# Optimization experiments

Hardware: AMD Instinct MI355X
Metric: run time of the kernel (lower is better)

## Reference

```python
import jax, jax.numpy as jnp
import numpy as np

B = 1024          # number of graphs
H = 8             # heads
EPS = 1e-5        # LayerNorm eps (torch default)
MEAN_RES_SCALE = 0.2


def _ln(x, w, b):
    mu = x.mean(-1, keepdims=True)
    var = ((x - mu) ** 2).mean(-1, keepdims=True)
    return (x - mu) / jnp.sqrt(var + EPS) * w + b


def setup_inputs() -> dict:
    key = jax.random.key(0)
    ks = jax.random.split(key, 10)
    N, D = 262144, 256
    s = 1.0 / np.sqrt(D)
    return {
        "h": jax.random.normal(ks[0], (N, D), jnp.float32),
        "batch": jnp.sort(jax.random.randint(ks[1], (N,), 0, B)),
        "cdr_mask": jax.random.bernoulli(ks[2], 0.2, (N,)),
        "iface_mask": jax.random.bernoulli(ks[3], 0.2, (N,)),
        "ln_kv_w": jnp.ones((D,), jnp.float32),
        "ln_kv_b": jnp.zeros((D,), jnp.float32),
        "ln_q_w": jnp.ones((D,), jnp.float32),
        "ln_q_b": jnp.zeros((D,), jnp.float32),
        "Wk": jax.random.normal(ks[4], (D, D), jnp.float32) * s,
        "Wv": jax.random.normal(ks[5], (D, D), jnp.float32) * s,
        "Wq": jax.random.normal(ks[6], (D, 2 * D), jnp.float32) * (1.0 / np.sqrt(2 * D)),
        "Wres": jax.random.normal(ks[7], (D, D), jnp.float32) * s,
        "Wout": jax.random.normal(ks[8], (D, D), jnp.float32) * s,
        "cdr_bias": jnp.asarray(0.6, jnp.float32),
        "iface_bias": jnp.asarray(0.8, jnp.float32),
        "logit_scale": jnp.asarray(1.0, jnp.float32),
    }


def reference(h, batch, cdr_mask, iface_mask, ln_kv_w, ln_kv_b, ln_q_w, ln_q_b,
              Wk, Wv, Wq, Wres, Wout, cdr_bias, iface_bias, logit_scale):
    N, D = h.shape
    hd = D // H
    # per-graph mean / max pooling (segment reductions; all segments non-empty)
    counts = jax.ops.segment_sum(jnp.ones((N,), h.dtype), batch, num_segments=B)[:, None]
    mean_raw = jax.ops.segment_sum(h, batch, num_segments=B) / counts      # [B,D]
    max_raw = jax.ops.segment_max(h, batch, num_segments=B)                # [B,D]
    # single query per graph (dropout = identity in eval)
    q = jnp.concatenate([mean_raw, max_raw], axis=-1) @ Wq.T               # [B,D]
    q = _ln(q, ln_q_w, ln_q_b).reshape(B, H, hd)                           # [B,H,hd]
    # keys / values per node
    h_ln = _ln(h, ln_kv_w, ln_kv_b)
    k = (h_ln @ Wk.T).reshape(N, H, hd)
    v = (h_ln @ Wv.T).reshape(N, H, hd)
    # attention logits with mask biases
    logit = (k * q[batch]).sum(-1) * (logit_scale / np.sqrt(hd))           # [N,H]
    logit = logit + cdr_bias * cdr_mask.astype(h.dtype)[:, None]
    logit = logit + iface_bias * iface_mask.astype(h.dtype)[:, None]
    # segment softmax over nodes of each graph
    m = jax.ops.segment_max(logit, batch, num_segments=B)                  # [B,H]
    e = jnp.exp(logit - m[batch])
    z = jax.ops.segment_sum(e, batch, num_segments=B)                      # [B,H]
    attn = e / z[batch]                                                    # [N,H]
    g = jax.ops.segment_sum(attn[..., None] * v, batch, num_segments=B)    # [B,H,hd]
    g = g.reshape(B, D)
    return g @ Wout.T + MEAN_RES_SCALE * (mean_raw @ Wres.T)               # [B,D]
```

## Files before the change

kernel.cpp:

```cpp
#include <hip/hip_runtime.h>

__global__ void k_offsets(const int* __restrict__ batch, int* __restrict__ start,
                          int N, int B) {
    int i = blockIdx.x * blockDim.x + threadIdx.x;
    if (i >= N) return;
    int b = batch[i];
    if (i == 0) {
        for (int g = 0; g <= b; ++g) start[g] = 0;
    } else {
        int pb = batch[i - 1];
        for (int g = pb + 1; g <= b; ++g) start[g] = i;
    }
    if (i == N - 1) {
        for (int g = b + 1; g <= B; ++g) start[g] = N;
    }
}

__global__ __launch_bounds__(256) void k_pool_q(
    const float* __restrict__ h, const int* __restrict__ start,
    const float* __restrict__ Wq, const float* __restrict__ Wk,
    const float* __restrict__ ln_q_w, const float* __restrict__ ln_q_b,
    const float* __restrict__ ln_kv_w, const float* __restrict__ logit_scale,
    float* __restrict__ mean_raw, float* __restrict__ w_eff)
{
    const int g = blockIdx.x;
    const int tid = threadIdx.x;
    const int w = tid >> 6;
    const int l = tid & 63;
    const int d = tid;
    const int s = start[g], e = start[g + 1];

    float4 sm = make_float4(0.f, 0.f, 0.f, 0.f);
    float4 mx = make_float4(-INFINITY, -INFINITY, -INFINITY, -INFINITY);
    int n = s + w;
    for (; n + 4 < e; n += 8) {
        const float4 a = *(const float4*)(h + (size_t)n * 256 + l * 4);
        const float4 b = *(const float4*)(h + (size_t)(n + 4) * 256 + l * 4);
        sm.x += a.x + b.x; sm.y += a.y + b.y; sm.z += a.z + b.z; sm.w += a.w + b.w;
        mx.x = fmaxf(mx.x, fmaxf(a.x, b.x)); mx.y = fmaxf(mx.y, fmaxf(a.y, b.y));
        mx.z = fmaxf(mx.z, fmaxf(a.z, b.z)); mx.w = fmaxf(mx.w, fmaxf(a.w, b.w));
    }
    if (n < e) {
        const float4 a = *(const float4*)(h + (size_t)n * 256 + l * 4);
        sm.x += a.x; sm.y += a.y; sm.z += a.z; sm.w += a.w;
        mx.x = fmaxf(mx.x, a.x); mx.y = fmaxf(mx.y, a.y);
        mx.z = fmaxf(mx.z, a.z); mx.w = fmaxf(mx.w, a.w);
    }

    __shared__ __align__(16) float PS[4][256];
    __shared__ __align__(16) float PM[4][256];
    *(float4*)(&PS[w][l * 4]) = sm;
    *(float4*)(&PM[w][l * 4]) = mx;
    __syncthreads();
    const float sum = (PS[0][d] + PS[1][d]) + (PS[2][d] + PS[3][d]);
    const float mxv = fmaxf(fmaxf(PM[0][d], PM[1][d]), fmaxf(PM[2][d], PM[3][d]));
    const float mean = sum / (float)(e - s);
    mean_raw[(size_t)g * 256 + d] = mean;

    __shared__ __align__(16) float X[512];
    __shared__ float QL[256];
    __shared__ float rs[4], rq[4];
    X[d] = mean;
    X[256 + d] = mxv;
    __syncthreads();

    float q = 0.f;
    const float* wqr = Wq + (size_t)d * 512;
    #pragma unroll 8
    for (int j = 0; j < 512; j += 4) {
        float4 w4 = *(const float4*)(wqr + j);
        q += w4.x * X[j] + w4.y * X[j + 1] + w4.z * X[j + 2] + w4.w * X[j + 3];
    }
    float s1 = q, s2 = q * q;
    #pragma unroll
    for (int off = 1; off < 64; off <<= 1) {
        s1 += __shfl_xor(s1, off);
        s2 += __shfl_xor(s2, off);
    }
    if ((d & 63) == 0) { rs[d >> 6] = s1; rq[d >> 6] = s2; }
    __syncthreads();
    const float t1 = rs[0] + rs[1] + rs[2] + rs[3];
    const float t2 = rq[0] + rq[1] + rq[2] + rq[3];
    const float mu = t1 * (1.f / 256.f);
    const float var = t2 * (1.f / 256.f) - mu * mu;
    const float rstd = rsqrtf(var + 1e-5f);
    QL[d] = (q - mu) * rstd * ln_q_w[d] + ln_q_b[d];
    __syncthreads();

    const float scale = logit_scale[0] * 0.17677669529663687f;
    const float fold = scale * ln_kv_w[d];
    #pragma unroll
    for (int hh = 0; hh < 8; ++hh) {
        float a = 0.f;
        #pragma unroll 8
        for (int r = 0; r < 32; ++r) {
            a += Wk[(size_t)(hh * 32 + r) * 256 + d] * QL[hh * 32 + r];
        }
        w_eff[((size_t)g * 8 + hh) * 256 + d] = a * fold;
    }
}

__global__ __launch_bounds__(256) void k_attn(
    const float* __restrict__ h, const int* __restrict__ start,
    const int* __restrict__ cdr, const int* __restrict__ ifm,
    const float* __restrict__ ln_w, const float* __restrict__ ln_b,
    const float* __restrict__ w_eff,
    const float* __restrict__ cdr_bias, const float* __restrict__ iface_bias,
    float* __restrict__ u_norm)
{
    const int g = blockIdx.x;
    const int tid = threadIdx.x;
    const int w = tid >> 6;
    const int l = tid & 63;
    const int hh = l >> 3;
    const int p = l & 7;
    const int s = start[g], e = start[g + 1];
    const float cb = cdr_bias[0], ib = iface_bias[0];

    float we[32];
    {
        const float* wp = w_eff + ((size_t)g * 8 + hh) * 256 + p * 32;
        #pragma unroll
        for (int r = 0; r < 8; ++r) {
            float4 t = *(const float4*)(wp + r * 4);
            we[4 * r + 0] = t.x; we[4 * r + 1] = t.y; we[4 * r + 2] = t.z; we[4 * r + 3] = t.w;
        }
    }
    float s1h = 0.f;
    #pragma unroll
    for (int r = 0; r < 32; ++r) s1h += we[r];
    s1h += __shfl_xor(s1h, 1);
    s1h += __shfl_xor(s1h, 2);
    s1h += __shfl_xor(s1h, 4);

    float m = -INFINITY, z = 0.f, sw = 0.f;
    float u[32];
    #pragma unroll
    for (int r = 0; r < 32; ++r) u[r] = 0.f;

    __shared__ __align__(16) float hbuf[4][288];
    __shared__ __align__(16) float UF[4][8][264];
    __shared__ float MW[4][8], ZW[4][8], SW[4][8], FG[4][8], IZ[8], SG[8];

    const int wofs = l * 4 + ((l >> 3) << 2);
    const int rofs = p * 36;

    int n = s + w;
    float4 xn = make_float4(0.f, 0.f, 0.f, 0.f);
    int cn = 0, im = 0;
    if (n < e) {
        xn = *(const float4*)(h + (size_t)n * 256 + l * 4);
        cn = cdr[n]; im = ifm[n];
    }
    while (n < e) {
        const float4 xc = xn;
        const int cc = cn, ic = im;
        const int n2 = n + 4;
        if (n2 < e) {
            xn = *(const float4*)(h + (size_t)n2 * 256 + l * 4);
            cn = cdr[n2]; im = ifm[n2];
        }

        *(float4*)(&hbuf[w][wofs]) = xc;
        asm volatile("s_waitcnt lgkmcnt(0)" ::: "memory");

        float hv[32];
        #pragma unroll
        for (int r = 0; r < 8; ++r) {
            float4 t = *(const float4*)(&hbuf[w][rofs + r * 4]);
            hv[4 * r + 0] = t.x; hv[4 * r + 1] = t.y; hv[4 * r + 2] = t.z; hv[4 * r + 3] = t.w;
        }
        float s1 = 0.f, s2 = 0.f, dt = 0.f;
        #pragma unroll
        for (int r = 0; r < 32; ++r) {
            const float v = hv[r];
            s1 += v;
            s2 = fmaf(v, v, s2);
            dt = fmaf(v, we[r], dt);
        }
        #pragma unroll
        for (int off = 1; off < 8; off <<= 1) {
            s1 += __shfl_xor(s1, off);
            s2 += __shfl_xor(s2, off);
            dt += __shfl_xor(dt, off);
        }
        const float mu = s1 * (1.f / 256.f);
        const float var = s2 * (1.f / 256.f) - mu * mu;
        const float rstd = rsqrtf(var + 1e-5f);
        const float mb = cb * (float)cc + ib * (float)ic;
        const float lv = rstd * (dt - mu * s1h) + mb;

        const float nm = fmaxf(m, lv);
        const float ee = __expf(lv - nm);
        const float c = ee * rstd;
        if (__any(lv > m)) {
            const float a = __expf(m - nm);
            z = z * a + ee;
            sw = sw * a + c * mu;
            #pragma unroll
            for (int r = 0; r < 32; ++r) u[r] = u[r] * a + c * hv[r];
            m = nm;
        } else {
            z += ee;
            sw += c * mu;
            #pragma unroll
            for (int r = 0; r < 32; ++r) u[r] = fmaf(c, hv[r], u[r]);
        }
        n = n2;
    }

    if (p == 0) { MW[w][hh] = m; ZW[w][hh] = z; SW[w][hh] = sw; }
    #pragma unroll
    for (int r = 0; r < 8; ++r) {
        float4 t = make_float4(u[4 * r], u[4 * r + 1], u[4 * r + 2], u[4 * r + 3]);
        *(float4*)(&UF[w][hh][p * 32 + r * 4]) = t;
    }
    __syncthreads();

    if (tid < 8) {
        const float mg = fmaxf(fmaxf(MW[0][tid], MW[1][tid]),
                               fmaxf(MW[2][tid], MW[3][tid]));
        float zg = 0.f, sg = 0.f;
        #pragma unroll
        for (int ww = 0; ww < 4; ++ww) {
            const float f = __expf(MW[ww][tid] - mg);
            FG[ww][tid] = f;
            zg += ZW[ww][tid] * f;
            sg += SW[ww][tid] * f;
        }
        IZ[tid] = 1.f / zg;
        SG[tid] = sg;
    }
    __syncthreads();

    const float lwj = ln_w[tid], lbj = ln_b[tid];
    #pragma unroll
    for (int h2 = 0; h2 < 8; ++h2) {
        const float Uv = UF[0][h2][tid] * FG[0][h2] + UF[1][h2][tid] * FG[1][h2]
                       + UF[2][h2][tid] * FG[2][h2] + UF[3][h2][tid] * FG[3][h2];
        u_norm[(size_t)g * 2048 + h2 * 256 + tid] = (Uv - SG[h2]) * IZ[h2] * lwj + lbj;
    }
}

__global__ __launch_bounds__(256) void k_out(
    const float* __restrict__ u_norm, const float* __restrict__ mean_raw,
    const float* __restrict__ Wv, const float* __restrict__ Wout,
    const float* __restrict__ Wres, float* __restrict__ out)
{
    const int d = threadIdx.x;
    const int g = blockIdx.x;
    __shared__ __align__(16) float UN[8][256];
    __shared__ __align__(16) float MR[256];
    __shared__ __align__(16) float GF[256];

    const float4* up = (const float4*)(u_norm + (size_t)g * 2048);
    ((float4*)UN)[d] = up[d];
    ((float4*)UN)[256 + d] = up[256 + d];
    if (d < 64) ((float4*)MR)[d] = ((const float4*)(mean_raw + (size_t)g * 256))[d];
    __syncthreads();

    const int hh = d >> 5;
    float acc = 0.f;
    const float* wvr = Wv + (size_t)d * 256;
    #pragma unroll 8
    for (int j = 0; j < 256; j += 4) {
        const float4 wv = *(const float4*)(wvr + j);
        const float4 uv = *(const float4*)(&UN[hh][j]);
        acc += wv.x * uv.x + wv.y * uv.y + wv.z * uv.z + wv.w * uv.w;
    }
    GF[d] = acc;
    __syncthreads();

    float oo = 0.f, rr = 0.f;
    const float* wor = Wout + (size_t)d * 256;
    const float* wrr = Wres + (size_t)d * 256;
    #pragma unroll 8
    for (int j = 0; j < 256; j += 4) {
        const float4 wo = *(const float4*)(wor + j);
        const float4 wq = *(const float4*)(wrr + j);
        const float4 gf = *(const float4*)(&GF[j]);
        const float4 mr = *(const float4*)(&MR[j]);
        oo += wo.x * gf.x + wo.y * gf.y + wo.z * gf.z + wo.w * gf.w;
        rr += wq.x * mr.x + wq.y * mr.y + wq.z * mr.z + wq.w * mr.w;
    }
    out[(size_t)g * 256 + d] = oo + 0.2f * rr;
}

extern "C" void kernel_launch(void* const* d_in, const int* in_sizes, int n_in,
                              void* d_out, int out_size, void* d_ws, size_t ws_size,
                              hipStream_t stream)
{
    const float* h        = (const float*)d_in[0];
    const int*   batch    = (const int*)d_in[1];
    const int*   cdr      = (const int*)d_in[2];
    const int*   ifm      = (const int*)d_in[3];
    const float* ln_kv_w  = (const float*)d_in[4];
    const float* ln_kv_b  = (const float*)d_in[5];
    const float* ln_q_w   = (const float*)d_in[6];
    const float* ln_q_b   = (const float*)d_in[7];
    const float* Wk       = (const float*)d_in[8];
    const float* Wv       = (const float*)d_in[9];
    const float* Wq       = (const float*)d_in[10];
    const float* Wres     = (const float*)d_in[11];
    const float* Wout     = (const float*)d_in[12];
    const float* cdr_b    = (const float*)d_in[13];
    const float* if_b     = (const float*)d_in[14];
    const float* lsc      = (const float*)d_in[15];

    const int N = in_sizes[0] / 256;
    const int B = out_size / 256;

    int*   start    = (int*)d_ws;
    float* mean_raw = (float*)((char*)d_ws + 8192);
    float* w_eff    = mean_raw + (size_t)B * 256;
    float* u_norm   = w_eff + (size_t)B * 2048;

    k_offsets<<<(N + 255) / 256, 256, 0, stream>>>(batch, start, N, B);
    k_pool_q<<<B, 256, 0, stream>>>(h, start, Wq, Wk, ln_q_w, ln_q_b, ln_kv_w, lsc,
                                    mean_raw, w_eff);
    k_attn<<<B, 256, 0, stream>>>(h, start, cdr, ifm, ln_kv_w, ln_kv_b, w_eff,
                                  cdr_b, if_b, u_norm);
    k_out<<<B, 256, 0, stream>>>(u_norm, mean_raw, Wv, Wout, Wres, (float*)d_out);
}
```

Baseline: 669.6 us.

## Split pooling into node-chunked atomic kernel, precompute mask bias, deepen attn prefetch

Mean/max pooling moves out of the per-graph q kernel into a separate kernel over fixed 128-node chunks. It accumulates per-graph partial sums and maxes with float atomicAdd and an ordered-int atomicMax, so load balance no longer depends on segment sizes. The mask bias is precomputed per node in the offsets kernel, and the attention loop now prefetches three rows ahead instead of one. This adds an init kernel, atomic traffic and extra launches, and float atomic summation makes the mean order-nondeterministic.

```diff
diff --git a/kernel.cpp b/kernel.cpp
--- a/kernel.cpp
+++ b/kernel.cpp
@@ -1,9 +1,27 @@
 #include <hip/hip_runtime.h>
 
-__global__ void k_offsets(const int* __restrict__ batch, int* __restrict__ start,
+__device__ __forceinline__ int okey(float x) {
+    int ix = __float_as_int(x);
+    return ix >= 0 ? ix : (ix ^ 0x7fffffff);
+}
+__device__ __forceinline__ float okey_dec(int k) {
+    return __int_as_float(k >= 0 ? k : (k ^ 0x7fffffff));
+}
+
+__global__ __launch_bounds__(256) void k_init(float* __restrict__ gsum,
+                                              int* __restrict__ gmax, int total) {
+    int i = blockIdx.x * blockDim.x + threadIdx.x;
+    if (i < total) { gsum[i] = 0.f; gmax[i] = (int)0x80000000; }
+}
+
+__global__ void k_offsets(const int* __restrict__ batch, const int* __restrict__ cdr,
+                          const int* __restrict__ ifm, const float* __restrict__ cdr_bias,
+                          const float* __restrict__ iface_bias,
+                          int* __restrict__ start, float* __restrict__ mbias,
                           int N, int B) {
     int i = blockIdx.x * blockDim.x + threadIdx.x;
     if (i >= N) return;
+    mbias[i] = cdr_bias[0] * (float)cdr[i] + iface_bias[0] * (float)ifm[i];
     int b = batch[i];
     if (i == 0) {
         for (int g = 0; g <= b; ++g) start[g] = 0;
@@ -16,45 +34,73 @@
     }
 }
 
-__global__ __launch_bounds__(256) void k_pool_q(
-    const float* __restrict__ h, const int* __restrict__ start,
+__global__ __launch_bounds__(256) void k_pool(
+    const float* __restrict__ h, const int* __restrict__ batch,
+    float* __restrict__ gsum, int* __restrict__ gmax, int N)
+{
+    const int c0 = blockIdx.x * 128;
+    const int tid = threadIdx.x;
+    const int w = tid >> 6;
+    const int l = tid & 63;
+    const int lim = min(128, N - c0);
+
+    __shared__ int bb[128];
+    if (tid < 128 && c0 + tid < N) bb[tid] = batch[c0 + tid];
+    __syncthreads();
+
+    float4 sm = make_float4(0.f, 0.f, 0.f, 0.f);
+    float4 mxv = make_float4(-INFINITY, -INFINITY, -INFINITY, -INFINITY);
+
+    const bool any = (w < lim);
+    int cur = any ? bb[w] : 0;
+
+    auto flush = [&](int g2) {
+        float* sp = gsum + ((size_t)g2 << 8) + (l << 2);
+        atomicAdd(sp + 0, sm.x); atomicAdd(sp + 1, sm.y);
+        atomicAdd(sp + 2, sm.z); atomicAdd(sp + 3, sm.w);
+        int* mp = gmax + ((size_t)g2 << 8) + (l << 2);
+        atomicMax(mp + 0, okey(mxv.x)); atomicMax(mp + 1, okey(mxv.y));
+        atomicMax(mp + 2, okey(mxv.z)); atomicMax(mp + 3, okey(mxv.w));
+    };
+
+    float4 xa = make_float4(0.f, 0.f, 0.f, 0.f);
+    float4 xb = make_float4(0.f, 0.f, 0.f, 0.f);
+    if (w < lim)     xa = *(const float4*)(h + (size_t)(c0 + w) * 256 + l * 4);
+    if (w + 4 < lim) xb = *(const float4*)(h + (size_t)(c0 + w + 4) * 256 + l * 4);
+
+    for (int idx = w; idx < lim; idx += 4) {
+        const float4 xc = xa;
+        xa = xb;
+        if (idx + 8 < lim)
+            xb = *(const float4*)(h + (size_t)(c0 + idx + 8) * 256 + l * 4);
+        const int bg = bb[idx];
+        if (bg != cur) {
+            flush(cur);
+            sm = make_float4(0.f, 0.f, 0.f, 0.f);
+            mxv = make_float4(-INFINITY, -INFINITY, -INFINITY, -INFINITY);
+            cur = bg;
+        }
+        sm.x += xc.x; sm.y += xc.y; sm.z += xc.z; sm.w += xc.w;
+        mxv.x = fmaxf(mxv.x, xc.x); mxv.y = fmaxf(mxv.y, xc.y);
+        mxv.z = fmaxf(mxv.z, xc.z); mxv.w = fmaxf(mxv.w, xc.w);
+    }
+    if (any) flush(cur);
+}
+
+__global__ __launch_bounds__(256) void k_q(
+    const float* __restrict__ gsum, const int* __restrict__ gmax,
+    const int* __restrict__ start,
     const float* __restrict__ Wq, const float* __restrict__ Wk,
     const float* __restrict__ ln_q_w, const float* __restrict__ ln_q_b,
     const float* __restrict__ ln_kv_w, const float* __restrict__ logit_scale,
     float* __restrict__ mean_raw, float* __restrict__ w_eff)
 {
     const int g = blockIdx.x;
-    const int tid = threadIdx.x;
-    const int w = tid >> 6;
-    const int l = tid & 63;
-    const int d = tid;
+    const int d = threadIdx.x;
     const int s = start[g], e = start[g + 1];
 
-    float4 sm = make_float4(0.f, 0.f, 0.f, 0.f);
-    float4 mx = make_float4(-INFINITY, -INFINITY, -INFINITY, -INFINITY);
-    int n = s + w;
-    for (; n + 4 < e; n += 8) {
-        const float4 a = *(const float4*)(h + (size_t)n * 256 + l * 4);
-        const float4 b = *(const float4*)(h + (size_t)(n + 4) * 256 + l * 4);
-        sm.x += a.x + b.x; sm.y += a.y + b.y; sm.z += a.z + b.z; sm.w += a.w + b.w;
-        mx.x = fmaxf(mx.x, fmaxf(a.x, b.x)); mx.y = fmaxf(mx.y, fmaxf(a.y, b.y));
-        mx.z = fmaxf(mx.z, fmaxf(a.z, b.z)); mx.w = fmaxf(mx.w, fmaxf(a.w, b.w));
-    }
-    if (n < e) {
-        const float4 a = *(const float4*)(h + (size_t)n * 256 + l * 4);
-        sm.x += a.x; sm.y += a.y; sm.z += a.z; sm.w += a.w;
-        mx.x = fmaxf(mx.x, a.x); mx.y = fmaxf(mx.y, a.y);
-        mx.z = fmaxf(mx.z, a.z); mx.w = fmaxf(mx.w, a.w);
-    }
-
-    __shared__ __align__(16) float PS[4][256];
-    __shared__ __align__(16) float PM[4][256];
-    *(float4*)(&PS[w][l * 4]) = sm;
-    *(float4*)(&PM[w][l * 4]) = mx;
-    __syncthreads();
-    const float sum = (PS[0][d] + PS[1][d]) + (PS[2][d] + PS[3][d]);
-    const float mxv = fmaxf(fmaxf(PM[0][d], PM[1][d]), fmaxf(PM[2][d], PM[3][d]));
-    const float mean = sum / (float)(e - s);
+    const float mean = gsum[(size_t)g * 256 + d] / (float)(e - s);
+    const float mxv = okey_dec(gmax[(size_t)g * 256 + d]);
     mean_raw[(size_t)g * 256 + d] = mean;
 
     __shared__ __align__(16) float X[512];
@@ -102,10 +148,9 @@
 
 __global__ __launch_bounds__(256) void k_attn(
     const float* __restrict__ h, const int* __restrict__ start,
-    const int* __restrict__ cdr, const int* __restrict__ ifm,
+    const float* __restrict__ mbias,
     const float* __restrict__ ln_w, const float* __restrict__ ln_b,
     const float* __restrict__ w_eff,
-    const float* __restrict__ cdr_bias, const float* __restrict__ iface_bias,
     float* __restrict__ u_norm)
 {
     const int g = blockIdx.x;
@@ -115,7 +160,6 @@
     const int hh = l >> 3;
     const int p = l & 7;
     const int s = start[g], e = start[g + 1];
-    const float cb = cdr_bias[0], ib = iface_bias[0];
 
     float we[32];
     {
@@ -145,25 +189,9 @@
     const int wofs = l * 4 + ((l >> 3) << 2);
     const int rofs = p * 36;
 
-    int n = s + w;
-    float4 xn = make_float4(0.f, 0.f, 0.f, 0.f);
-    int cn = 0, im = 0;
-    if (n < e) {
-        xn = *(const float4*)(h + (size_t)n * 256 + l * 4);
-        cn = cdr[n]; im = ifm[n];
-    }
-    while (n < e) {
-        const float4 xc = xn;
-        const int cc = cn, ic = im;
-        const int n2 = n + 4;
-        if (n2 < e) {
-            xn = *(const float4*)(h + (size_t)n2 * 256 + l * 4);
-            cn = cdr[n2]; im = ifm[n2];
-        }
-
+    auto process = [&](const float4& xc, float mbv) {
         *(float4*)(&hbuf[w][wofs]) = xc;
         asm volatile("s_waitcnt lgkmcnt(0)" ::: "memory");
-
         float hv[32];
         #pragma unroll
         for (int r = 0; r < 8; ++r) {
@@ -187,8 +215,7 @@
         const float mu = s1 * (1.f / 256.f);
         const float var = s2 * (1.f / 256.f) - mu * mu;
         const float rstd = rsqrtf(var + 1e-5f);
-        const float mb = cb * (float)cc + ib * (float)ic;
-        const float lv = rstd * (dt - mu * s1h) + mb;
+        const float lv = rstd * (dt - mu * s1h) + mbv;
 
         const float nm = fmaxf(m, lv);
         const float ee = __expf(lv - nm);
@@ -206,7 +233,27 @@
             #pragma unroll
             for (int r = 0; r < 32; ++r) u[r] = fmaf(c, hv[r], u[r]);
         }
-        n = n2;
+    };
+
+    int n = s + w;
+    float4 x0 = make_float4(0.f, 0.f, 0.f, 0.f);
+    float4 x1 = x0, x2 = x0;
+    float b0 = 0.f, b1 = 0.f, b2 = 0.f;
+    if (n < e)     { x0 = *(const float4*)(h + (size_t)n * 256 + l * 4);        b0 = mbias[n]; }
+    if (n + 4 < e) { x1 = *(const float4*)(h + (size_t)(n + 4) * 256 + l * 4);  b1 = mbias[n + 4]; }
+    if (n + 8 < e) { x2 = *(const float4*)(h + (size_t)(n + 8) * 256 + l * 4);  b2 = mbias[n + 8]; }
+
+    for (; n < e; n += 12) {
+        process(x0, b0);
+        if (n + 12 < e) { x0 = *(const float4*)(h + (size_t)(n + 12) * 256 + l * 4); b0 = mbias[n + 12]; }
+        if (n + 4 < e) {
+            process(x1, b1);
+            if (n + 16 < e) { x1 = *(const float4*)(h + (size_t)(n + 16) * 256 + l * 4); b1 = mbias[n + 16]; }
+            if (n + 8 < e) {
+                process(x2, b2);
+                if (n + 20 < e) { x2 = *(const float4*)(h + (size_t)(n + 20) * 256 + l * 4); b2 = mbias[n + 20]; }
+            }
+        }
     }
 
     if (p == 0) { MW[w][hh] = m; ZW[w][hh] = z; SW[w][hh] = sw; }
@@ -314,11 +361,16 @@
     float* mean_raw = (float*)((char*)d_ws + 8192);
     float* w_eff    = mean_raw + (size_t)B * 256;
     float* u_norm   = w_eff + (size_t)B * 2048;
-
-    k_offsets<<<(N + 255) / 256, 256, 0, stream>>>(batch, start, N, B);
-    k_pool_q<<<B, 256, 0, stream>>>(h, start, Wq, Wk, ln_q_w, ln_q_b, ln_kv_w, lsc,
-                                    mean_raw, w_eff);
-    k_attn<<<B, 256, 0, stream>>>(h, start, cdr, ifm, ln_kv_w, ln_kv_b, w_eff,
-                                  cdr_b, if_b, u_norm);
+    float* gsum     = u_norm + (size_t)B * 2048;
+    int*   gmax     = (int*)(gsum + (size_t)B * 256);
+    float* mbias    = (float*)(gmax + (size_t)B * 256);
+
+    k_init<<<(B * 256 + 255) / 256, 256, 0, stream>>>(gsum, gmax, B * 256);
+    k_offsets<<<(N + 255) / 256, 256, 0, stream>>>(batch, cdr, ifm, cdr_b, if_b,
+                                                   start, mbias, N, B);
+    k_pool<<<(N + 127) / 128, 256, 0, stream>>>(h, batch, gsum, gmax, N);
+    k_q<<<B, 256, 0, stream>>>(gsum, gmax, start, Wq, Wk, ln_q_w, ln_q_b, ln_kv_w,
+                               lsc, mean_raw, w_eff);
+    k_attn<<<B, 256, 0, stream>>>(h, start, mbias, ln_kv_w, ln_kv_b, w_eff, u_norm);
     k_out<<<B, 256, 0, stream>>>(u_norm, mean_raw, Wv, Wout, Wres, (float*)d_out);
 }
```

Result: slower. 711.3 us (+6.2%).

## Split per-graph pooling across four blocks and precompute mask biases

Applied to the files above, without the earlier changes.

Pooling is moved out of the fused pool+query kernel into its own kernel with four blocks per graph. Each block reduces a quarter of the graph's nodes into partial sum and max buffers, which a new query kernel then combines. The aim is more memory-level parallelism for the bandwidth-bound streaming pass over h. It also precomputes a per-node float mask bias in the offsets kernel, so the attention loop loads one float instead of two ints. This costs an extra kernel launch plus extra workspace traffic for the partials and bias array.

```diff
diff --git a/kernel.cpp b/kernel.cpp
--- a/kernel.cpp
+++ b/kernel.cpp
@@ -1,9 +1,13 @@
 #include <hip/hip_runtime.h>
 
-__global__ void k_offsets(const int* __restrict__ batch, int* __restrict__ start,
+__global__ void k_offsets(const int* __restrict__ batch, const int* __restrict__ cdr,
+                          const int* __restrict__ ifm, const float* __restrict__ cdr_bias,
+                          const float* __restrict__ iface_bias,
+                          int* __restrict__ start, float* __restrict__ mbias,
                           int N, int B) {
     int i = blockIdx.x * blockDim.x + threadIdx.x;
     if (i >= N) return;
+    mbias[i] = cdr_bias[0] * (float)cdr[i] + iface_bias[0] * (float)ifm[i];
     int b = batch[i];
     if (i == 0) {
         for (int g = 0; g <= b; ++g) start[g] = 0;
@@ -16,44 +20,73 @@
     }
 }
 
-__global__ __launch_bounds__(256) void k_pool_q(
+__global__ __launch_bounds__(256) void k_pool(
     const float* __restrict__ h, const int* __restrict__ start,
+    float* __restrict__ psum, float* __restrict__ pmax)
+{
+    const int g = blockIdx.x >> 2;
+    const int sl = blockIdx.x & 3;
+    const int tid = threadIdx.x;
+    const int w = tid >> 6;
+    const int l = tid & 63;
+    const int s = start[g], e = start[g + 1];
+    const int len = e - s;
+    const int qs = s + (len * sl) / 4;
+    const int qe = s + (len * (sl + 1)) / 4;
+
+    float4 sm = make_float4(0.f, 0.f, 0.f, 0.f);
+    float4 mx = make_float4(-INFINITY, -INFINITY, -INFINITY, -INFINITY);
+
+    int n = qs + w;
+    for (; n + 12 < qe; n += 16) {
+        const float4 a = *(const float4*)(h + (size_t)n * 256 + l * 4);
+        const float4 b = *(const float4*)(h + (size_t)(n + 4) * 256 + l * 4);
+        const float4 c = *(const float4*)(h + (size_t)(n + 8) * 256 + l * 4);
+        const float4 d4 = *(const float4*)(h + (size_t)(n + 12) * 256 + l * 4);
+        sm.x += (a.x + b.x) + (c.x + d4.x); sm.y += (a.y + b.y) + (c.y + d4.y);
+        sm.z += (a.z + b.z) + (c.z + d4.z); sm.w += (a.w + b.w) + (c.w + d4.w);
+        mx.x = fmaxf(mx.x, fmaxf(fmaxf(a.x, b.x), fmaxf(c.x, d4.x)));
+        mx.y = fmaxf(mx.y, fmaxf(fmaxf(a.y, b.y), fmaxf(c.y, d4.y)));
+        mx.z = fmaxf(mx.z, fmaxf(fmaxf(a.z, b.z), fmaxf(c.z, d4.z)));
+        mx.w = fmaxf(mx.w, fmaxf(fmaxf(a.w, b.w), fmaxf(c.w, d4.w)));
+    }
+    for (; n < qe; n += 4) {
+        const float4 a = *(const float4*)(h + (size_t)n * 256 + l * 4);
+        sm.x += a.x; sm.y += a.y; sm.z += a.z; sm.w += a.w;
+        mx.x = fmaxf(mx.x, a.x); mx.y = fmaxf(mx.y, a.y);
+        mx.z = fmaxf(mx.z, a.z); mx.w = fmaxf(mx.w, a.w);
+    }
+
+    __shared__ __align__(16) float PS[4][256];
+    __shared__ __align__(16) float PM[4][256];
+    *(float4*)(&PS[w][l * 4]) = sm;
+    *(float4*)(&PM[w][l * 4]) = mx;
+    __syncthreads();
+    const int d = tid;
+    const float sum = (PS[0][d] + PS[1][d]) + (PS[2][d] + PS[3][d]);
+    const float mxv = fmaxf(fmaxf(PM[0][d], PM[1][d]), fmaxf(PM[2][d], PM[3][d]));
+    psum[(size_t)blockIdx.x * 256 + d] = sum;
+    pmax[(size_t)blockIdx.x * 256 + d] = mxv;
+}
+
+__global__ __launch_bounds__(256) void k_q(
+    const float* __restrict__ psum, const float* __restrict__ pmax,
+    const int* __restrict__ start,
     const float* __restrict__ Wq, const float* __restrict__ Wk,
     const float* __restrict__ ln_q_w, const float* __restrict__ ln_q_b,
     const float* __restrict__ ln_kv_w, const float* __restrict__ logit_scale,
     float* __restrict__ mean_raw, float* __restrict__ w_eff)
 {
     const int g = blockIdx.x;
-    const int tid = threadIdx.x;
-    const int w = tid >> 6;
-    const int l = tid & 63;
-    const int d = tid;
+    const int d = threadIdx.x;
     const int s = start[g], e = start[g + 1];
 
-    float4 sm = make_float4(0.f, 0.f, 0.f, 0.f);
-    float4 mx = make_float4(-INFINITY, -INFINITY, -INFINITY, -INFINITY);
-    int n = s + w;
-    for (; n + 4 < e; n += 8) {
-        const float4 a = *(const float4*)(h + (size_t)n * 256 + l * 4);
-        const float4 b = *(const float4*)(h + (size_t)(n + 4) * 256 + l * 4);
-        sm.x += a.x + b.x; sm.y += a.y + b.y; sm.z += a.z + b.z; sm.w += a.w + b.w;
-        mx.x = fmaxf(mx.x, fmaxf(a.x, b.x)); mx.y = fmaxf(mx.y, fmaxf(a.y, b.y));
-        mx.z = fmaxf(mx.z, fmaxf(a.z, b.z)); mx.w = fmaxf(mx.w, fmaxf(a.w, b.w));
-    }
-    if (n < e) {
-        const float4 a = *(const float4*)(h + (size_t)n * 256 + l * 4);
-        sm.x += a.x; sm.y += a.y; sm.z += a.z; sm.w += a.w;
-        mx.x = fmaxf(mx.x, a.x); mx.y = fmaxf(mx.y, a.y);
-        mx.z = fmaxf(mx.z, a.z); mx.w = fmaxf(mx.w, a.w);
-    }
-
-    __shared__ __align__(16) float PS[4][256];
-    __shared__ __align__(16) float PM[4][256];
-    *(float4*)(&PS[w][l * 4]) = sm;
-    *(float4*)(&PM[w][l * 4]) = mx;
-    __syncthreads();
-    const float sum = (PS[0][d] + PS[1][d]) + (PS[2][d] + PS[3][d]);
-    const float mxv = fmaxf(fmaxf(PM[0][d], PM[1][d]), fmaxf(PM[2][d], PM[3][d]));
+    float sum = 0.f, mxv = -INFINITY;
+    #pragma unroll
+    for (int sl = 0; sl < 4; ++sl) {
+        sum += psum[((size_t)g * 4 + sl) * 256 + d];
+        mxv = fmaxf(mxv, pmax[((size_t)g * 4 + sl) * 256 + d]);
+    }
     const float mean = sum / (float)(e - s);
     mean_raw[(size_t)g * 256 + d] = mean;
 
@@ -102,10 +135,9 @@
 
 __global__ __launch_bounds__(256) void k_attn(
     const float* __restrict__ h, const int* __restrict__ start,
-    const int* __restrict__ cdr, const int* __restrict__ ifm,
+    const float* __restrict__ mbias,
     const float* __restrict__ ln_w, const float* __restrict__ ln_b,
     const float* __restrict__ w_eff,
-    const float* __restrict__ cdr_bias, const float* __restrict__ iface_bias,
     float* __restrict__ u_norm)
 {
     const int g = blockIdx.x;
@@ -115,7 +147,6 @@
     const int hh = l >> 3;
     const int p = l & 7;
     const int s = start[g], e = start[g + 1];
-    const float cb = cdr_bias[0], ib = iface_bias[0];
 
     float we[32];
     {
@@ -147,18 +178,18 @@
 
     int n = s + w;
     float4 xn = make_float4(0.f, 0.f, 0.f, 0.f);
-    int cn = 0, im = 0;
+    float bn = 0.f;
     if (n < e) {
         xn = *(const float4*)(h + (size_t)n * 256 + l * 4);
-        cn = cdr[n]; im = ifm[n];
+        bn = mbias[n];
     }
     while (n < e) {
         const float4 xc = xn;
-        const int cc = cn, ic = im;
+        const float bc = bn;
         const int n2 = n + 4;
         if (n2 < e) {
             xn = *(const float4*)(h + (size_t)n2 * 256 + l * 4);
-            cn = cdr[n2]; im = ifm[n2];
+            bn = mbias[n2];
         }
 
         *(float4*)(&hbuf[w][wofs]) = xc;
@@ -187,8 +218,7 @@
         const float mu = s1 * (1.f / 256.f);
         const float var = s2 * (1.f / 256.f) - mu * mu;
         const float rstd = rsqrtf(var + 1e-5f);
-        const float mb = cb * (float)cc + ib * (float)ic;
-        const float lv = rstd * (dt - mu * s1h) + mb;
+        const float lv = rstd * (dt - mu * s1h) + bc;
 
         const float nm = fmaxf(m, lv);
         const float ee = __expf(lv - nm);
@@ -314,11 +344,15 @@
     float* mean_raw = (float*)((char*)d_ws + 8192);
     float* w_eff    = mean_raw + (size_t)B * 256;
     float* u_norm   = w_eff + (size_t)B * 2048;
-
-    k_offsets<<<(N + 255) / 256, 256, 0, stream>>>(batch, start, N, B);
-    k_pool_q<<<B, 256, 0, stream>>>(h, start, Wq, Wk, ln_q_w, ln_q_b, ln_kv_w, lsc,
-                                    mean_raw, w_eff);
-    k_attn<<<B, 256, 0, stream>>>(h, start, cdr, ifm, ln_kv_w, ln_kv_b, w_eff,
-                                  cdr_b, if_b, u_norm);
+    float* psum     = u_norm + (size_t)B * 2048;
+    float* pmax     = psum + (size_t)B * 1024;
+    float* mbias    = pmax + (size_t)B * 1024;
+
+    k_offsets<<<(N + 255) / 256, 256, 0, stream>>>(batch, cdr, ifm, cdr_b, if_b,
+                                                   start, mbias, N, B);
+    k_pool<<<B * 4, 256, 0, stream>>>(h, start, psum, pmax);
+    k_q<<<B, 256, 0, stream>>>(psum, pmax, start, Wq, Wk, ln_q_w, ln_q_b, ln_kv_w,
+                               lsc, mean_raw, w_eff);
+    k_attn<<<B, 256, 0, stream>>>(h, start, mbias, ln_kv_w, ln_kv_b, w_eff, u_norm);
     k_out<<<B, 256, 0, stream>>>(u_norm, mean_raw, Wv, Wout, Wres, (float*)d_out);
 }
```

New measurement: 663.7 us. No clear change (-0.9%).
